# Performance work log

Hardware: AMD Instinct MI355X
Metric: run time of the kernel (lower is better)

## Reference

```python
import jax, jax.numpy as jnp
import numpy as np

EPS = 1e-12

def t5_layer_norm(x, w):
    # T5-style RMS norm: no mean subtraction, no bias
    var = jnp.mean(x * x, axis=-1, keepdims=True)
    return x * jax.lax.rsqrt(var + EPS) * w

def gether(h, a2, t2):
    # a2: [B,S,1,1] (row similarity), t2: [B,1,S,1] (col similarity)
    h_y = h * t2
    h_left  = jnp.pad(h_y, ((0,0),(0,0),(1,0),(0,0)))[:, :, :-1, :]
    h_right = jnp.pad(h_y, ((0,0),(0,0),(0,1),(0,0)))[:, :, 1:, :]
    h_x = h * a2
    h_up   = jnp.pad(h_x, ((0,0),(1,0),(0,0),(0,0)))[:, :-1, :, :]
    h_down = jnp.pad(h_x, ((0,0),(0,1),(0,0),(0,0)))[:, 1:, :, :]
    return h + h_left + h_right + h_up + h_down

def syntax_gether(h, dep_weights):
    h_dep = h * dep_weights            # [B,S,S,D]
    h_in = jnp.sum(h_dep, axis=2)      # [B,S,D]
    h_out = jnp.sum(h_dep, axis=1)     # [B,S,D]
    return h_in[:, :, None, :] + h_out[:, None, :, :]

def feature_fusion(sem, syn, gate_w, gate_b):
    combined = jnp.concatenate([sem, syn], axis=-1)
    gate = jax.nn.sigmoid(combined @ gate_w + gate_b)
    return gate * sem + (1.0 - gate) * syn

def setup_inputs() -> dict:
    key = jax.random.key(0)
    ks = jax.random.split(key, 16)
    B, S, D_in, D_out = 4, 96, 768, 256
    N_DEP, D_DEP = 44, 6
    inp = {
        "table": jax.random.normal(ks[0], (B, S, S, D_in), dtype=jnp.float32),
        "a_simi": jax.random.uniform(ks[1], (B, S), dtype=jnp.float32),
        "t_simi": jax.random.uniform(ks[2], (B, S), dtype=jnp.float32),
        "dep_matrix": jax.random.randint(ks[3], (B, S, S), 0, 2).astype(jnp.float32),
        "dep_types": jax.random.randint(ks[4], (B, S, S), 0, N_DEP).astype(jnp.int32),
        # parameters (torch Linear weights stored transposed: [in, out])
        "dense1_w": jax.random.normal(ks[5], (D_in, D_in), dtype=jnp.float32) * 0.02,
        "dense1_b": jnp.zeros((D_in,), dtype=jnp.float32),
        "dense2_w": jax.random.normal(ks[6], (D_in, D_out), dtype=jnp.float32) * 0.02,
        "dense2_b": jnp.zeros((D_out,), dtype=jnp.float32),
        "dep_emb": jax.random.normal(ks[7], (N_DEP, D_DEP), dtype=jnp.float32) * 0.02,
        "dep_att_w": jax.random.normal(ks[8], (D_DEP, 1), dtype=jnp.float32) * 0.02,
        "dep_att_b": jnp.zeros((1,), dtype=jnp.float32),
        "gate_w": jax.random.normal(ks[9], (2 * D_in, D_in), dtype=jnp.float32) * 0.02,
        "gate_b": jnp.zeros((D_in,), dtype=jnp.float32),
        "norm1_w": jnp.ones((D_in,), dtype=jnp.float32),
        "norm2_w": jnp.ones((D_out,), dtype=jnp.float32),
    }
    return inp

def reference(table, a_simi, t_simi, dep_matrix, dep_types,
              dense1_w, dense1_b, dense2_w, dense2_b,
              dep_emb, dep_att_w, dep_att_b, gate_w, gate_b,
              norm1_w, norm2_w):
    a2 = a_simi[:, :, None, None]   # [B,S,1,1]
    t2 = t_simi[:, None, :, None]   # [B,1,S,1]
    dep_embeds = dep_emb[dep_types]                       # [B,S,S,6]
    dep_weights = jax.nn.sigmoid(dep_embeds @ dep_att_w + dep_att_b)
    dep_weights = dep_weights * dep_matrix[..., None]     # [B,S,S,1]

    h0 = table
    h1_sem = gether(h0, a2, t2)
    h1_syn = syntax_gether(h0, dep_weights)
    h1 = feature_fusion(h1_sem, h1_syn, gate_w, gate_b)
    h1 = jax.nn.relu(t5_layer_norm((h1 + h0) @ dense1_w + dense1_b, norm1_w))

    h2_sem = gether(h1, a2, t2)
    h2_syn = syntax_gether(h1, dep_weights)
    h2 = feature_fusion(h2_sem, h2_syn, gate_w, gate_b)
    h2 = jax.nn.relu(t5_layer_norm((h2 + h1) @ dense2_w + dense2_b, norm2_w))
    return h2
```

## Files before the change

### kernel.cpp

```cpp
#include <hip/hip_runtime.h>
#include <cstdint>
#include <cstddef>

#define SDIM 96
#define BDIM 4
#define NROWS (BDIM * SDIM * SDIM)
#define BSROWS (BDIM * SDIM)
#define DIN 768
#define DOUT 256

typedef short s16x8 __attribute__((ext_vector_type(8)));
typedef float f32x4 __attribute__((ext_vector_type(4)));
typedef unsigned short ushort_t;
typedef unsigned int uint_t;

__device__ __forceinline__ float sigmoid_f(float x) { return 1.0f / (1.0f + expf(-x)); }

__device__ __forceinline__ ushort_t f2bf(float x) {
    uint_t u = __float_as_uint(x);
    u = u + 0x7fffu + ((u >> 16) & 1u);
    return (ushort_t)(u >> 16);
}
__device__ __forceinline__ float bf2f(ushort_t h) {
    return __uint_as_float(((uint_t)h) << 16);
}

__device__ __forceinline__ void split_store(float x, ushort_t* __restrict__ ph,
                                            ushort_t* __restrict__ pl) {
    ushort_t h = f2bf(x);
    *ph = h;
    *pl = f2bf(x - bf2f(h));
}

__device__ __forceinline__ void load_lds16(const void* g, void* l) {
    __builtin_amdgcn_global_load_lds((const __attribute__((address_space(1))) uint_t*)g,
                                     (__attribute__((address_space(3))) uint_t*)l, 16, 0, 0);
}

__global__ __launch_bounds__(256) void depw_k(const int* __restrict__ types,
                                              const float* __restrict__ dmat,
                                              const float* __restrict__ emb,
                                              const float* __restrict__ aw,
                                              const float* __restrict__ ab,
                                              float* __restrict__ Wd) {
    int idx = blockIdx.x * 256 + threadIdx.x;
    if (idx >= NROWS) return;
    int t = types[idx];
    float s = ab[0];
#pragma unroll
    for (int k = 0; k < 6; ++k) s = fmaf(emb[t * 6 + k], aw[k], s);
    Wd[idx] = dmat[idx] * sigmoid_f(s);
}

__global__ __launch_bounds__(256) void splitT_k(const float* __restrict__ W,
                                                ushort_t* __restrict__ TH,
                                                ushort_t* __restrict__ TL, int K, int N) {
    int k = blockIdx.x * 256 + threadIdx.x;
    int n = blockIdx.y;
    if (k >= K) return;
    float x = W[(size_t)k * N + n];
    split_store(x, &TH[(size_t)n * K + k], &TL[(size_t)n * K + k]);
}

__global__ __launch_bounds__(256) void rowsum_k(const float* __restrict__ h,
                                                const float* __restrict__ W,
                                                float* __restrict__ hinF,
                                                ushort_t* __restrict__ hinH,
                                                ushort_t* __restrict__ hinL) {
    int d = blockIdx.x * 256 + threadIdx.x;
    int bi = blockIdx.y;
    const float* hp = h + (size_t)bi * SDIM * DIN + d;
    const float* wp = W + bi * SDIM;
    float acc = 0.f;
#pragma unroll 8
    for (int j = 0; j < SDIM; ++j) acc = fmaf(wp[j], hp[(size_t)j * DIN], acc);
    size_t o = (size_t)bi * DIN + d;
    hinF[o] = acc;
    split_store(acc, &hinH[o], &hinL[o]);
}

__global__ __launch_bounds__(256) void colsum_k(const float* __restrict__ h,
                                                const float* __restrict__ W,
                                                float* __restrict__ houtF,
                                                ushort_t* __restrict__ houtH,
                                                ushort_t* __restrict__ houtL) {
    int d = blockIdx.x * 256 + threadIdx.x;
    int bj = blockIdx.y;
    int b = bj / SDIM;
    int j = bj - b * SDIM;
    const float* hp = h + ((size_t)(b * SDIM) * SDIM + j) * DIN + d;
    const float* wp = W + (size_t)(b * SDIM) * SDIM + j;
    float acc = 0.f;
#pragma unroll 8
    for (int i = 0; i < SDIM; ++i)
        acc = fmaf(wp[(size_t)i * SDIM], hp[(size_t)i * SDIM * DIN], acc);
    size_t o = (size_t)bj * DIN + d;
    houtF[o] = acc;
    split_store(acc, &houtH[o], &houtL[o]);
}

__global__ __launch_bounds__(256) void sem_k(const float* __restrict__ h,
                                             const float* __restrict__ a_simi,
                                             const float* __restrict__ t_simi,
                                             ushort_t* __restrict__ semH,
                                             ushort_t* __restrict__ semL) {
    int idx = blockIdx.x * 256 + threadIdx.x;
    int d4 = idx % 192;
    int m = idx / 192;
    int j = m % SDIM;
    int r = m / SDIM;
    int i = r % SDIM;
    int b = r / SDIM;
    const float4* h4 = (const float4*)h;
    float4 acc = h4[(size_t)m * 192 + d4];
    if (j > 0) {
        float t = t_simi[b * SDIM + j - 1];
        float4 v = h4[(size_t)(m - 1) * 192 + d4];
        acc.x = fmaf(t, v.x, acc.x); acc.y = fmaf(t, v.y, acc.y);
        acc.z = fmaf(t, v.z, acc.z); acc.w = fmaf(t, v.w, acc.w);
    }
    if (j < SDIM - 1) {
        float t = t_simi[b * SDIM + j + 1];
        float4 v = h4[(size_t)(m + 1) * 192 + d4];
        acc.x = fmaf(t, v.x, acc.x); acc.y = fmaf(t, v.y, acc.y);
        acc.z = fmaf(t, v.z, acc.z); acc.w = fmaf(t, v.w, acc.w);
    }
    if (i > 0) {
        float a = a_simi[b * SDIM + i - 1];
        float4 v = h4[(size_t)(m - SDIM) * 192 + d4];
        acc.x = fmaf(a, v.x, acc.x); acc.y = fmaf(a, v.y, acc.y);
        acc.z = fmaf(a, v.z, acc.z); acc.w = fmaf(a, v.w, acc.w);
    }
    if (i < SDIM - 1) {
        float a = a_simi[b * SDIM + i + 1];
        float4 v = h4[(size_t)(m + SDIM) * 192 + d4];
        acc.x = fmaf(a, v.x, acc.x); acc.y = fmaf(a, v.y, acc.y);
        acc.z = fmaf(a, v.z, acc.z); acc.w = fmaf(a, v.w, acc.w);
    }
    size_t o = (size_t)m * DIN + d4 * 4;
    ushort_t hh[4], ll[4];
    float vv[4] = {acc.x, acc.y, acc.z, acc.w};
#pragma unroll
    for (int e = 0; e < 4; ++e) {
        hh[e] = f2bf(vv[e]);
        ll[e] = f2bf(vv[e] - bf2f(hh[e]));
    }
    *(ushort4*)&semH[o] = make_ushort4(hh[0], hh[1], hh[2], hh[3]);
    *(ushort4*)&semL[o] = make_ushort4(ll[0], ll[1], ll[2], ll[3]);
}

template <int EPI>
__global__ __launch_bounds__(256) void gemm_mfma(
    const ushort_t* __restrict__ AH, const ushort_t* __restrict__ AL,
    const ushort_t* __restrict__ BH, const ushort_t* __restrict__ BL,
    int M, int N, int K, int nbx,
    float* __restrict__ C, const float* __restrict__ bias,
    ushort_t* __restrict__ XH, ushort_t* __restrict__ XL,
    const float* __restrict__ Pin, const float* __restrict__ Pout,
    const float* __restrict__ hin, const float* __restrict__ hout,
    const float* __restrict__ hprev) {
    __shared__ __align__(16) ushort_t Ash[128 * 32];
    __shared__ __align__(16) ushort_t Asl[128 * 32];
    __shared__ __align__(16) ushort_t Bsh[128 * 32];
    __shared__ __align__(16) ushort_t Bsl[128 * 32];

    const int nwg = gridDim.x;
    const int orig = blockIdx.x;
    const int qq = nwg >> 3, rr = nwg & 7;
    const int xcd = orig & 7, sidx = orig >> 3;
    const int swz = (xcd < rr ? xcd * (qq + 1) : rr * (qq + 1) + (xcd - rr) * qq) + sidx;
    const int bx = swz % nbx;
    const int by = swz / nbx;
    const int bm = by * 128, bn = bx * 128;

    const int tid = threadIdx.x;
    const int wave = tid >> 6, lane = tid & 63;
    const int laneRow = lane >> 2;
    const int laneKB = (lane & 3) * 8;
    const int g = lane >> 4, q = lane & 15;
    const int wm = wave >> 1, wn = wave & 1;

    f32x4 acc[4][4];
#pragma unroll
    for (int a = 0; a < 4; ++a)
#pragma unroll
        for (int b = 0; b < 4; ++b) acc[a][b] = (f32x4){0.f, 0.f, 0.f, 0.f};

    for (int k0 = 0; k0 < K; k0 += 32) {
        __syncthreads();
#pragma unroll
        for (int cc = 0; cc < 2; ++cc) {
            const int c = wave + cc * 4;
            const int row = c * 16 + laneRow;
            const size_t ga = (size_t)(bm + row) * K + k0 + laneKB;
            const size_t gb = (size_t)(bn + row) * K + k0 + laneKB;
            char* la = (char*)Ash + c * 1024;
            char* lb = (char*)Bsh + c * 1024;
            load_lds16(AH + ga, la);
            load_lds16(AL + ga, (char*)Asl + c * 1024);
            load_lds16(BH + gb, lb);
            load_lds16(BL + gb, (char*)Bsl + c * 1024);
        }
        __syncthreads();

        s16x8 ah[4], al[4], bh[4], bl[4];
#pragma unroll
        for (int f = 0; f < 4; ++f) {
            const int ar = (wm * 64 + f * 16 + q) * 32 + g * 8;
            const int br = (wn * 64 + f * 16 + q) * 32 + g * 8;
            ah[f] = *(const s16x8*)&Ash[ar];
            al[f] = *(const s16x8*)&Asl[ar];
            bh[f] = *(const s16x8*)&Bsh[br];
            bl[f] = *(const s16x8*)&Bsl[br];
        }
#pragma unroll
        for (int mf = 0; mf < 4; ++mf)
#pragma unroll
            for (int nf = 0; nf < 4; ++nf) {
                acc[mf][nf] = __builtin_amdgcn_mfma_f32_16x16x32_bf16(ah[mf], bh[nf], acc[mf][nf], 0, 0, 0);
                acc[mf][nf] = __builtin_amdgcn_mfma_f32_16x16x32_bf16(ah[mf], bl[nf], acc[mf][nf], 0, 0, 0);
                acc[mf][nf] = __builtin_amdgcn_mfma_f32_16x16x32_bf16(al[mf], bh[nf], acc[mf][nf], 0, 0, 0);
            }
    }

#pragma unroll
    for (int mf = 0; mf < 4; ++mf) {
#pragma unroll
        for (int jj = 0; jj < 4; ++jj) {
            const int gr = bm + wm * 64 + mf * 16 + g * 4 + jj;
            int ri = 0, rj = 0;
            if (EPI == 1) {
                const int b_ = gr / 9216;
                const int rem = gr - b_ * 9216;
                const int i_ = rem / 96;
                const int j_ = rem - i_ * 96;
                ri = (b_ * 96 + i_) * 768;
                rj = (b_ * 96 + j_) * 768;
            }
#pragma unroll
            for (int nf = 0; nf < 4; ++nf) {
                const int gc = bn + wn * 64 + nf * 16 + q;
                float v = acc[mf][nf][jj];
                if (EPI == 0) {
                    if (bias != nullptr) v += bias[gc];
                    C[(size_t)gr * N + gc] = v;
                } else {
                    const float gte = sigmoid_f(v + Pin[ri + gc] + Pout[rj + gc]);
                    const float syn = hin[ri + gc] + hout[rj + gc];
                    const size_t o = (size_t)gr * 768 + gc;
                    const float sem = bf2f(AH[o]) + bf2f(AL[o]);
                    const float x = fmaf(gte, sem - syn, syn) + hprev[o];
                    split_store(x, &XH[o], &XL[o]);
                }
            }
        }
    }
}

template <int D>
__global__ __launch_bounds__(256) void norm_relu_k(const float* __restrict__ Y,
                                                   const float* __restrict__ w,
                                                   float* __restrict__ out) {
    constexpr int E = D / 256;
    int row = blockIdx.x;
    int tid = threadIdx.x;
    float v[E];
    float ss = 0.f;
#pragma unroll
    for (int e = 0; e < E; ++e) {
        v[e] = Y[(size_t)row * D + e * 256 + tid];
        ss = fmaf(v[e], v[e], ss);
    }
#pragma unroll
    for (int off = 32; off >= 1; off >>= 1) ss += __shfl_down(ss, off);
    __shared__ float red[4];
    int lane = tid & 63;
    int wid = tid >> 6;
    if (lane == 0) red[wid] = ss;
    __syncthreads();
    float tot = red[0] + red[1] + red[2] + red[3];
    float scale = rsqrtf(tot / (float)D + 1e-12f);
#pragma unroll
    for (int e = 0; e < E; ++e) {
        float o = v[e] * scale * w[e * 256 + tid];
        out[(size_t)row * D + e * 256 + tid] = fmaxf(o, 0.f);
    }
}

extern "C" void kernel_launch(void* const* d_in, const int* in_sizes, int n_in,
                              void* d_out, int out_size, void* d_ws, size_t ws_size,
                              hipStream_t stream) {
    (void)in_sizes; (void)n_in; (void)out_size; (void)ws_size;
    const float* table = (const float*)d_in[0];
    const float* a_simi = (const float*)d_in[1];
    const float* t_simi = (const float*)d_in[2];
    const float* dep_matrix = (const float*)d_in[3];
    const int* dep_types = (const int*)d_in[4];
    const float* d1w = (const float*)d_in[5];
    const float* d1b = (const float*)d_in[6];
    const float* d2w = (const float*)d_in[7];
    const float* d2b = (const float*)d_in[8];
    const float* dep_emb = (const float*)d_in[9];
    const float* att_w = (const float*)d_in[10];
    const float* att_b = (const float*)d_in[11];
    const float* gate_w = (const float*)d_in[12];
    const float* gate_b = (const float*)d_in[13];
    const float* nw1 = (const float*)d_in[14];
    const float* nw2 = (const float*)d_in[15];
    float* out = (float*)d_out;

    char* ws = (char*)d_ws;
    size_t off = 0;
    float* Wd = (float*)(ws + off); off += 147456;
    float* hinF = (float*)(ws + off); off += 1179648;
    float* houtF = (float*)(ws + off); off += 1179648;
    float* Pin = (float*)(ws + off); off += 1179648;
    float* Pout = (float*)(ws + off); off += 1179648;
    ushort_t* hinH = (ushort_t*)(ws + off); off += 589824;
    ushort_t* hinL = (ushort_t*)(ws + off); off += 589824;
    ushort_t* houtH = (ushort_t*)(ws + off); off += 589824;
    ushort_t* houtL = (ushort_t*)(ws + off); off += 589824;
    ushort_t* GtopTH = (ushort_t*)(ws + off); off += 1179648;
    ushort_t* GtopTL = (ushort_t*)(ws + off); off += 1179648;
    ushort_t* GbotTH = (ushort_t*)(ws + off); off += 1179648;
    ushort_t* GbotTL = (ushort_t*)(ws + off); off += 1179648;
    ushort_t* D1TH = (ushort_t*)(ws + off); off += 1179648;
    ushort_t* D1TL = (ushort_t*)(ws + off); off += 1179648;
    ushort_t* D2TH = (ushort_t*)(ws + off); off += 393216;
    ushort_t* D2TL = (ushort_t*)(ws + off); off += 393216;
    char* P1 = ws + off; off += 113246208;
    char* P2 = ws + off; off += 113246208;
    char* P3 = ws + off; off += 113246208;

    const size_t HALF = 56623104;
    ushort_t* S1H = (ushort_t*)P1;            ushort_t* S1L = (ushort_t*)(P1 + HALF);
    ushort_t* X1H = (ushort_t*)P2;            ushort_t* X1L = (ushort_t*)(P2 + HALF);
    float* Y1 = (float*)P1;
    float* h1 = (float*)P3;
    ushort_t* S2H = (ushort_t*)P2;            ushort_t* S2L = (ushort_t*)(P2 + HALF);
    ushort_t* X2H = (ushort_t*)P1;            ushort_t* X2L = (ushort_t*)(P1 + HALF);
    float* Y2 = (float*)P3;

    const dim3 blk(256);
    const dim3 gSplit768(3, 768);
    const dim3 gSplit256(3, 256);
    const dim3 gRS(DIN / 256, BSROWS);
    const int gSem = (NROWS * (DIN / 4)) / 256;
    const int gBig = (NROWS / 128) * (DIN / 128);
    const int gD2g = (NROWS / 128) * (DOUT / 128);
    const int gP = (BSROWS / 128) * (DIN / 128);

    depw_k<<<NROWS / 256, blk, 0, stream>>>(dep_types, dep_matrix, dep_emb, att_w, att_b, Wd);
    splitT_k<<<gSplit768, blk, 0, stream>>>(gate_w, GtopTH, GtopTL, DIN, DIN);
    splitT_k<<<gSplit768, blk, 0, stream>>>(gate_w + (size_t)DIN * DIN, GbotTH, GbotTL, DIN, DIN);
    splitT_k<<<gSplit768, blk, 0, stream>>>(d1w, D1TH, D1TL, DIN, DIN);
    splitT_k<<<gSplit256, blk, 0, stream>>>(d2w, D2TH, D2TL, DIN, DOUT);

    rowsum_k<<<gRS, blk, 0, stream>>>(table, Wd, hinF, hinH, hinL);
    colsum_k<<<gRS, blk, 0, stream>>>(table, Wd, houtF, houtH, houtL);
    sem_k<<<gSem, blk, 0, stream>>>(table, a_simi, t_simi, S1H, S1L);
    gemm_mfma<0><<<gP, blk, 0, stream>>>(hinH, hinL, GbotTH, GbotTL, BSROWS, DIN, DIN, DIN / 128,
                                         Pin, gate_b, nullptr, nullptr, nullptr, nullptr, nullptr, nullptr, nullptr);
    gemm_mfma<0><<<gP, blk, 0, stream>>>(houtH, houtL, GbotTH, GbotTL, BSROWS, DIN, DIN, DIN / 128,
                                         Pout, nullptr, nullptr, nullptr, nullptr, nullptr, nullptr, nullptr, nullptr);
    gemm_mfma<1><<<gBig, blk, 0, stream>>>(S1H, S1L, GtopTH, GtopTL, NROWS, DIN, DIN, DIN / 128,
                                           nullptr, nullptr, X1H, X1L, Pin, Pout, hinF, houtF, table);
    gemm_mfma<0><<<gBig, blk, 0, stream>>>(X1H, X1L, D1TH, D1TL, NROWS, DIN, DIN, DIN / 128,
                                           Y1, d1b, nullptr, nullptr, nullptr, nullptr, nullptr, nullptr, nullptr);
    norm_relu_k<DIN><<<NROWS, blk, 0, stream>>>(Y1, nw1, h1);

    rowsum_k<<<gRS, blk, 0, stream>>>(h1, Wd, hinF, hinH, hinL);
    colsum_k<<<gRS, blk, 0, stream>>>(h1, Wd, houtF, houtH, houtL);
    sem_k<<<gSem, blk, 0, stream>>>(h1, a_simi, t_simi, S2H, S2L);
    gemm_mfma<0><<<gP, blk, 0, stream>>>(hinH, hinL, GbotTH, GbotTL, BSROWS, DIN, DIN, DIN / 128,
                                         Pin, gate_b, nullptr, nullptr, nullptr, nullptr, nullptr, nullptr, nullptr);
    gemm_mfma<0><<<gP, blk, 0, stream>>>(houtH, houtL, GbotTH, GbotTL, BSROWS, DIN, DIN, DIN / 128,
                                         Pout, nullptr, nullptr, nullptr, nullptr, nullptr, nullptr, nullptr, nullptr);
    gemm_mfma<1><<<gBig, blk, 0, stream>>>(S2H, S2L, GtopTH, GtopTL, NROWS, DIN, DIN, DIN / 128,
                                           nullptr, nullptr, X2H, X2L, Pin, Pout, hinF, houtF, h1);
    gemm_mfma<0><<<gD2g, blk, 0, stream>>>(X2H, X2L, D2TH, D2TL, NROWS, DOUT, DIN, DOUT / 128,
                                           Y2, d2b, nullptr, nullptr, nullptr, nullptr, nullptr, nullptr, nullptr);
    norm_relu_k<DOUT><<<NROWS, blk, 0, stream>>>(Y2, nw2, out);
}
```

Baseline: 1.302 ms.

## Double-buffer LDS tiles in split-bf16 MFMA GEMM and reorder LDS layout

Converts the GEMM main loop to a two-stage LDS ping-pong: the next K-tile's global-to-LDS loads are issued before the current tile's MFMAs, and one barrier per iteration replaces two. It also changes the lane-to-row mapping so each lane loads and reads a contiguous 16-byte fragment (lane*8), which removes strided LDS reads and likely bank conflicts. s_setprio is raised around the MFMA block. LDS use doubles to 64KB per block, which may reduce occupancy.

```diff
diff --git a/kernel.cpp b/kernel.cpp
--- a/kernel.cpp
+++ b/kernel.cpp
@@ -159,10 +159,10 @@
     const float* __restrict__ Pin, const float* __restrict__ Pout,
     const float* __restrict__ hin, const float* __restrict__ hout,
     const float* __restrict__ hprev) {
-    __shared__ __align__(16) ushort_t Ash[128 * 32];
-    __shared__ __align__(16) ushort_t Asl[128 * 32];
-    __shared__ __align__(16) ushort_t Bsh[128 * 32];
-    __shared__ __align__(16) ushort_t Bsl[128 * 32];
+    __shared__ __align__(16) ushort_t Ash[2][4096];
+    __shared__ __align__(16) ushort_t Asl[2][4096];
+    __shared__ __align__(16) ushort_t Bsh[2][4096];
+    __shared__ __align__(16) ushort_t Bsl[2][4096];
 
     const int nwg = gridDim.x;
     const int orig = blockIdx.x;
@@ -175,9 +175,8 @@
 
     const int tid = threadIdx.x;
     const int wave = tid >> 6, lane = tid & 63;
-    const int laneRow = lane >> 2;
-    const int laneKB = (lane & 3) * 8;
-    const int g = lane >> 4, q = lane & 15;
+    const int lq = lane & 15;
+    const int lg = lane >> 4;
     const int wm = wave >> 1, wn = wave & 1;
 
     f32x4 acc[4][4];
@@ -186,33 +185,40 @@
 #pragma unroll
         for (int b = 0; b < 4; ++b) acc[a][b] = (f32x4){0.f, 0.f, 0.f, 0.f};
 
-    for (int k0 = 0; k0 < K; k0 += 32) {
-        __syncthreads();
-#pragma unroll
-        for (int cc = 0; cc < 2; ++cc) {
-            const int c = wave + cc * 4;
-            const int row = c * 16 + laneRow;
-            const size_t ga = (size_t)(bm + row) * K + k0 + laneKB;
-            const size_t gb = (size_t)(bn + row) * K + k0 + laneKB;
-            char* la = (char*)Ash + c * 1024;
-            char* lb = (char*)Bsh + c * 1024;
-            load_lds16(AH + ga, la);
-            load_lds16(AL + ga, (char*)Asl + c * 1024);
-            load_lds16(BH + gb, lb);
-            load_lds16(BL + gb, (char*)Bsl + c * 1024);
+    const int nt = K >> 5;
+
+#define STAGE(buf, k0)                                                              \
+    {                                                                               \
+        _Pragma("unroll") for (int cc = 0; cc < 2; ++cc) {                          \
+            const int c = wave + cc * 4;                                            \
+            const int row = c * 16 + lq;                                            \
+            const size_t ga = (size_t)(bm + row) * K + (k0) + lg * 8;               \
+            const size_t gb = (size_t)(bn + row) * K + (k0) + lg * 8;               \
+            load_lds16(AH + ga, &Ash[buf][c * 512]);                                \
+            load_lds16(AL + ga, &Asl[buf][c * 512]);                                \
+            load_lds16(BH + gb, &Bsh[buf][c * 512]);                                \
+            load_lds16(BL + gb, &Bsl[buf][c * 512]);                                \
+        }                                                                           \
+    }
+
+    STAGE(0, 0);
+    __syncthreads();
+
+    int cur = 0;
+    for (int t = 0; t < nt; ++t) {
+        if (t + 1 < nt) STAGE(cur ^ 1, (t + 1) * 32);
+
+        s16x8 ah[4], al[4], bh[4], bl[4];
+#pragma unroll
+        for (int f = 0; f < 4; ++f) {
+            const int cA = (wm * 4 + f) * 512 + lane * 8;
+            const int cB = (wn * 4 + f) * 512 + lane * 8;
+            ah[f] = *(const s16x8*)&Ash[cur][cA];
+            al[f] = *(const s16x8*)&Asl[cur][cA];
+            bh[f] = *(const s16x8*)&Bsh[cur][cB];
+            bl[f] = *(const s16x8*)&Bsl[cur][cB];
         }
-        __syncthreads();
-
-        s16x8 ah[4], al[4], bh[4], bl[4];
-#pragma unroll
-        for (int f = 0; f < 4; ++f) {
-            const int ar = (wm * 64 + f * 16 + q) * 32 + g * 8;
-            const int br = (wn * 64 + f * 16 + q) * 32 + g * 8;
-            ah[f] = *(const s16x8*)&Ash[ar];
-            al[f] = *(const s16x8*)&Asl[ar];
-            bh[f] = *(const s16x8*)&Bsh[br];
-            bl[f] = *(const s16x8*)&Bsl[br];
-        }
+        __builtin_amdgcn_s_setprio(1);
 #pragma unroll
         for (int mf = 0; mf < 4; ++mf)
 #pragma unroll
@@ -221,13 +227,17 @@
                 acc[mf][nf] = __builtin_amdgcn_mfma_f32_16x16x32_bf16(ah[mf], bl[nf], acc[mf][nf], 0, 0, 0);
                 acc[mf][nf] = __builtin_amdgcn_mfma_f32_16x16x32_bf16(al[mf], bh[nf], acc[mf][nf], 0, 0, 0);
             }
-    }
+        __builtin_amdgcn_s_setprio(0);
+        __syncthreads();
+        cur ^= 1;
+    }
+#undef STAGE
 
 #pragma unroll
     for (int mf = 0; mf < 4; ++mf) {
 #pragma unroll
         for (int jj = 0; jj < 4; ++jj) {
-            const int gr = bm + wm * 64 + mf * 16 + g * 4 + jj;
+            const int gr = bm + wm * 64 + mf * 16 + lg * 4 + jj;
             int ri = 0, rj = 0;
             if (EPI == 1) {
                 const int b_ = gr / 9216;
@@ -239,7 +249,7 @@
             }
 #pragma unroll
             for (int nf = 0; nf < 4; ++nf) {
-                const int gc = bn + wn * 64 + nf * 16 + q;
+                const int gc = bn + wn * 64 + nf * 16 + lq;
                 float v = acc[mf][nf][jj];
                 if (EPI == 0) {
                     if (bias != nullptr) v += bias[gc];
```

After: 1.525 ms. +17.1%, slower.
